# Kernel tuning notes

Measured on AMD Instinct MI355X. Metric: run time of the kernel, lower is better.

## Reference

```python
import jax, jax.numpy as jnp
import numpy as np

S = 2        # downscale
REDUCE = 32  # QK channel dim


def _to_grid(x):
    # [B,C,H,W] -> [B,C,H/S,W/S,S*S], matching ConverToGrid (reshape+permute+reshape)
    B, C, H, W = x.shape
    h, w = H // S, W // S
    x = x.reshape(B, C, h, S, w, S)
    x = x.transpose(0, 1, 2, 4, 3, 5)
    return x.reshape(B, C, h, w, S * S)


def setup_inputs() -> dict:
    key = jax.random.key(0)
    k1, k2, k3 = jax.random.split(key, 3)
    fm = jax.random.normal(k1, (8, 128, 256, 256), dtype=jnp.float32)
    Wq = jax.random.normal(k2, (REDUCE, 128), dtype=jnp.float32) * 0.05
    Wk = jax.random.normal(k3, (REDUCE, 128), dtype=jnp.float32) * 0.05
    return {"fm": fm, "Wq": Wq, "Wk": Wk}


def reference(fm, Wq, Wk):
    B, C, H, W = fm.shape
    h, w = H // S, W // S
    # Q branch: AvgPool2d(S,S) -> 1x1 conv -> scale by 1/sqrt(reduce)
    pooled = fm.reshape(B, C, h, S, w, S).mean(axis=(3, 5))          # [B,C,h,w]
    Q = jnp.einsum('rc,bchw->brhw', Wq, pooled) / jnp.sqrt(
        jnp.asarray(REDUCE, fm.dtype))                               # [B,r,h,w]
    # K branch: 1x1 conv -> grid
    K = _to_grid(jnp.einsum('rc,bchw->brhw', Wk, fm))                # [B,r,h,w,S*S]
    # V branch: grid of raw features
    V = _to_grid(fm)                                                 # [B,C,h,w,S*S]
    # sum over channel dim of Q*K, softmax over window dim (dropout p=0 => identity)
    logits = jnp.einsum('brhw,brhws->bhws', Q, K)                    # [B,h,w,S*S]
    attn = jax.nn.softmax(logits, axis=-1)
    # weighted sum over window positions
    out = jnp.einsum('bchws,bhws->bchw', V, attn)                    # [B,C,h,w]
    return out
```

## Files before the change

### kernel.cpp

```cpp
#include <hip/hip_runtime.h>
#include <math.h>


__global__ __launch_bounds__(256) void wt_kernel(const float* __restrict__ Wq,
                                                 const float* __restrict__ Wk,
                                                 float* __restrict__ ws) {
  int t = blockIdx.x * 256 + threadIdx.x;
  if (t < 4096) {
    int c = t >> 5, r = t & 31;
    ws[c * 32 + r]        = Wq[r * 128 + c] * (0.25f / sqrtf(32.0f));
    ws[4096 + c * 32 + r] = Wk[r * 128 + c];
  }
}

__global__ __launch_bounds__(256, 8)
void attn_main(const float* __restrict__ fm,
               const float* __restrict__ ws,
               float* __restrict__ out) {
  __shared__ float Qpart[32 * 128];
  __shared__ float lbuf[2 * 128 * 4];

  const int tid  = threadIdx.x;
  const int p    = tid & 127;
  const int half = __builtin_amdgcn_readfirstlane(tid >> 7);
  const int blk  = blockIdx.x;
  const int h    = blk & 127;
  const int b    = blk >> 7;
  const int cbase = half * 64;

  const float* gbase = fm + ((size_t)(b * 128 + cbase) * 65536) +
                       (size_t)(2 * h) * 256 + 2 * p;
  const float* wq = ws + cbase * 32;
  const float* wk = ws + 4096 + cbase * 32;

  float qa[32];
#pragma unroll
  for (int r = 0; r < 32; ++r) qa[r] = 0.f;
  {
    const float* g = gbase;
#pragma unroll 4
    for (int i = 0; i < 64; ++i) {
      const float2 va = *(const float2*)(g);
      const float2 vb = *(const float2*)(g + 256);
      const float u = (va.x + va.y) + (vb.x + vb.y);
#pragma unroll
      for (int r = 0; r < 32; ++r)
        qa[r] = fmaf(wq[i * 32 + r], u, qa[r]);
      g += 65536;
    }
  }
  if (half == 1) {
#pragma unroll
    for (int r = 0; r < 32; ++r) Qpart[r * 128 + p] = qa[r];
  }
  __syncthreads();
  if (half == 0) {
#pragma unroll
    for (int r = 0; r < 32; ++r) {
      const float t = qa[r] + Qpart[r * 128 + p];
      qa[r] = t;
      Qpart[r * 128 + p] = t;
    }
  }
  __syncthreads();
  if (half == 1) {
#pragma unroll
    for (int r = 0; r < 32; ++r) qa[r] = Qpart[r * 128 + p];
  }

  float l0 = 0.f, l1 = 0.f, l2 = 0.f, l3 = 0.f;
  {
    const float* g = gbase + (size_t)63 * 65536;
#pragma unroll 2
    for (int i = 63; i >= 0; --i) {
      const float2 va = *(const float2*)(g);
      const float2 vb = *(const float2*)(g + 256);
      float t0 = 0.f, t1 = 0.f, t2 = 0.f, t3 = 0.f;
#pragma unroll
      for (int r = 0; r < 32; r += 4) {
        t0 = fmaf(qa[r + 0], wk[i * 32 + r + 0], t0);
        t1 = fmaf(qa[r + 1], wk[i * 32 + r + 1], t1);
        t2 = fmaf(qa[r + 2], wk[i * 32 + r + 2], t2);
        t3 = fmaf(qa[r + 3], wk[i * 32 + r + 3], t3);
      }
      const float tv = (t0 + t1) + (t2 + t3);
      l0 = fmaf(tv, va.x, l0);
      l1 = fmaf(tv, va.y, l1);
      l2 = fmaf(tv, vb.x, l2);
      l3 = fmaf(tv, vb.y, l3);
      g -= 65536;
    }
  }
  *(float4*)(lbuf + (half * 128 + p) * 4) = make_float4(l0, l1, l2, l3);
  __syncthreads();

  if (half == 0) {
    const float4 o = *(const float4*)(lbuf + (128 + p) * 4);
    const float L0 = l0 + o.x, L1 = l1 + o.y, L2 = l2 + o.z, L3 = l3 + o.w;
    const float mx = fmaxf(fmaxf(L0, L1), fmaxf(L2, L3));
    const float e0 = __expf(L0 - mx), e1 = __expf(L1 - mx);
    const float e2 = __expf(L2 - mx), e3 = __expf(L3 - mx);
    const float inv = 1.0f / ((e0 + e1) + (e2 + e3));
    *(float4*)(lbuf + p * 4) =
        make_float4(e0 * inv, e1 * inv, e2 * inv, e3 * inv);
  }
  __syncthreads();
  const float4 at = *(const float4*)(lbuf + p * 4);

  {
    const float* g = gbase;
    float* op = out + ((size_t)(b * 128 + cbase) * 16384) + h * 128 + p;
#pragma unroll 8
    for (int i = 0; i < 64; ++i) {
      const float2 va = *(const float2*)(g);
      const float2 vb = *(const float2*)(g + 256);
      const float o =
          fmaf(at.x, va.x, fmaf(at.y, va.y, fmaf(at.z, vb.x, at.w * vb.y)));
      __builtin_nontemporal_store(o, op);
      g += 65536;
      op += 16384;
    }
  }
}

extern "C" void kernel_launch(void* const* d_in, const int* in_sizes, int n_in,
                              void* d_out, int out_size, void* d_ws, size_t ws_size,
                              hipStream_t stream) {
  const float* fm = (const float*)d_in[0];
  const float* Wq = (const float*)d_in[1];
  const float* Wk = (const float*)d_in[2];
  float* outp = (float*)d_out;
  float* ws = (float*)d_ws;

  wt_kernel<<<16, 256, 0, stream>>>(Wq, Wk, ws);
  attn_main<<<1024, 256, 0, stream>>>(fm, ws, outp);
}
```

Measured before the change: 149.0 us.

## Split channels over four waves per block and halve row width per block

Each block now covers half a pooled row (64 columns) with four wavefronts, each owning 32 channels instead of 64. The grid doubles to 2048 blocks, and the Q and logit partial sums are reduced across four groups in shared memory. The channel loops are manually unrolled by four so several independent loads are in flight, which aims to raise memory-level parallelism and occupancy for this bandwidth-bound kernel. In exchange there is more reduction traffic through shared memory, and each wave's row segment is shorter, so global accesses are less contiguous.

```diff
diff --git a/kernel.cpp b/kernel.cpp
--- a/kernel.cpp
+++ b/kernel.cpp
@@ -17,86 +17,119 @@
 void attn_main(const float* __restrict__ fm,
                const float* __restrict__ ws,
                float* __restrict__ out) {
-  __shared__ float Qpart[32 * 128];
-  __shared__ float lbuf[2 * 128 * 4];
+  __shared__ float Qpart[2 * 32 * 64];
+  __shared__ float lbuf[4 * 64 * 4];
 
-  const int tid  = threadIdx.x;
-  const int p    = tid & 127;
-  const int half = __builtin_amdgcn_readfirstlane(tid >> 7);
-  const int blk  = blockIdx.x;
-  const int h    = blk & 127;
-  const int b    = blk >> 7;
-  const int cbase = half * 64;
+  const int tid = threadIdx.x;
+  const int p   = tid & 63;
+  const int grp = __builtin_amdgcn_readfirstlane(tid >> 6);
 
-  const float* gbase = fm + ((size_t)(b * 128 + cbase) * 65536) +
-                       (size_t)(2 * h) * 256 + 2 * p;
-  const float* wq = ws + cbase * 32;
-  const float* wk = ws + 4096 + cbase * 32;
+  const int blk = blockIdx.x;
+  const int w0  = (blk & 1) * 64;
+  const int h   = (blk >> 1) & 127;
+  const int b   = blk >> 8;
+  const int cb  = grp * 32;
+
+  const float* gbase = fm + ((size_t)(b * 128 + cb) * 65536) +
+                       (size_t)(2 * h) * 256 + 2 * (w0 + p);
+  const float* wq = ws + cb * 32;
+  const float* wk = ws + 4096 + cb * 32;
 
   float qa[32];
 #pragma unroll
   for (int r = 0; r < 32; ++r) qa[r] = 0.f;
   {
     const float* g = gbase;
-#pragma unroll 4
-    for (int i = 0; i < 64; ++i) {
-      const float2 va = *(const float2*)(g);
-      const float2 vb = *(const float2*)(g + 256);
-      const float u = (va.x + va.y) + (vb.x + vb.y);
+#pragma unroll 2
+    for (int i0 = 0; i0 < 32; i0 += 4) {
+      const float2 va0 = *(const float2*)(g + 0 * 65536);
+      const float2 vb0 = *(const float2*)(g + 0 * 65536 + 256);
+      const float2 va1 = *(const float2*)(g + 1 * 65536);
+      const float2 vb1 = *(const float2*)(g + 1 * 65536 + 256);
+      const float2 va2 = *(const float2*)(g + 2 * 65536);
+      const float2 vb2 = *(const float2*)(g + 2 * 65536 + 256);
+      const float2 va3 = *(const float2*)(g + 3 * 65536);
+      const float2 vb3 = *(const float2*)(g + 3 * 65536 + 256);
+      const float u0 = (va0.x + va0.y) + (vb0.x + vb0.y);
+      const float u1 = (va1.x + va1.y) + (vb1.x + vb1.y);
+      const float u2 = (va2.x + va2.y) + (vb2.x + vb2.y);
+      const float u3 = (va3.x + va3.y) + (vb3.x + vb3.y);
 #pragma unroll
-      for (int r = 0; r < 32; ++r)
-        qa[r] = fmaf(wq[i * 32 + r], u, qa[r]);
-      g += 65536;
+      for (int r = 0; r < 32; ++r) {
+        float acc = qa[r];
+        acc = fmaf(wq[(i0 + 0) * 32 + r], u0, acc);
+        acc = fmaf(wq[(i0 + 1) * 32 + r], u1, acc);
+        acc = fmaf(wq[(i0 + 2) * 32 + r], u2, acc);
+        acc = fmaf(wq[(i0 + 3) * 32 + r], u3, acc);
+        qa[r] = acc;
+      }
+      g += 4 * 65536;
     }
   }
-  if (half == 1) {
+
+  if (grp >= 2) {
 #pragma unroll
-    for (int r = 0; r < 32; ++r) Qpart[r * 128 + p] = qa[r];
+    for (int r = 0; r < 32; ++r) Qpart[(grp - 2) * 2048 + r * 64 + p] = qa[r];
   }
   __syncthreads();
-  if (half == 0) {
+  if (grp < 2) {
 #pragma unroll
     for (int r = 0; r < 32; ++r) {
-      const float t = qa[r] + Qpart[r * 128 + p];
-      qa[r] = t;
-      Qpart[r * 128 + p] = t;
+      const float t = qa[r] + Qpart[grp * 2048 + r * 64 + p];
+      Qpart[grp * 2048 + r * 64 + p] = t;
     }
   }
   __syncthreads();
-  if (half == 1) {
 #pragma unroll
-    for (int r = 0; r < 32; ++r) qa[r] = Qpart[r * 128 + p];
-  }
+  for (int r = 0; r < 32; ++r)
+    qa[r] = Qpart[r * 64 + p] + Qpart[2048 + r * 64 + p];
 
   float l0 = 0.f, l1 = 0.f, l2 = 0.f, l3 = 0.f;
   {
-    const float* g = gbase + (size_t)63 * 65536;
+    const float* g = gbase + (size_t)28 * 65536;
 #pragma unroll 2
-    for (int i = 63; i >= 0; --i) {
-      const float2 va = *(const float2*)(g);
-      const float2 vb = *(const float2*)(g + 256);
-      float t0 = 0.f, t1 = 0.f, t2 = 0.f, t3 = 0.f;
+    for (int i0 = 28; i0 >= 0; i0 -= 4) {
+      const float2 va0 = *(const float2*)(g + 0 * 65536);
+      const float2 vb0 = *(const float2*)(g + 0 * 65536 + 256);
+      const float2 va1 = *(const float2*)(g + 1 * 65536);
+      const float2 vb1 = *(const float2*)(g + 1 * 65536 + 256);
+      const float2 va2 = *(const float2*)(g + 2 * 65536);
+      const float2 vb2 = *(const float2*)(g + 2 * 65536 + 256);
+      const float2 va3 = *(const float2*)(g + 3 * 65536);
+      const float2 vb3 = *(const float2*)(g + 3 * 65536 + 256);
 #pragma unroll
-      for (int r = 0; r < 32; r += 4) {
-        t0 = fmaf(qa[r + 0], wk[i * 32 + r + 0], t0);
-        t1 = fmaf(qa[r + 1], wk[i * 32 + r + 1], t1);
-        t2 = fmaf(qa[r + 2], wk[i * 32 + r + 2], t2);
-        t3 = fmaf(qa[r + 3], wk[i * 32 + r + 3], t3);
+      for (int j = 0; j < 4; ++j) {
+        const int c = i0 + j;
+        float t0 = 0.f, t1 = 0.f, t2 = 0.f, t3 = 0.f;
+#pragma unroll
+        for (int r = 0; r < 32; r += 4) {
+          t0 = fmaf(qa[r + 0], wk[c * 32 + r + 0], t0);
+          t1 = fmaf(qa[r + 1], wk[c * 32 + r + 1], t1);
+          t2 = fmaf(qa[r + 2], wk[c * 32 + r + 2], t2);
+          t3 = fmaf(qa[r + 3], wk[c * 32 + r + 3], t3);
+        }
+        const float tv = (t0 + t1) + (t2 + t3);
+        const float2 va = (j == 0) ? va0 : (j == 1) ? va1 : (j == 2) ? va2 : va3;
+        const float2 vb = (j == 0) ? vb0 : (j == 1) ? vb1 : (j == 2) ? vb2 : vb3;
+        l0 = fmaf(tv, va.x, l0);
+        l1 = fmaf(tv, va.y, l1);
+        l2 = fmaf(tv, vb.x, l2);
+        l3 = fmaf(tv, vb.y, l3);
       }
-      const float tv = (t0 + t1) + (t2 + t3);
-      l0 = fmaf(tv, va.x, l0);
-      l1 = fmaf(tv, va.y, l1);
-      l2 = fmaf(tv, vb.x, l2);
-      l3 = fmaf(tv, vb.y, l3);
-      g -= 65536;
+      g -= 4 * 65536;
     }
   }
-  *(float4*)(lbuf + (half * 128 + p) * 4) = make_float4(l0, l1, l2, l3);
+  *(float4*)(lbuf + (grp * 64 + p) * 4) = make_float4(l0, l1, l2, l3);
   __syncthreads();
 
-  if (half == 0) {
-    const float4 o = *(const float4*)(lbuf + (128 + p) * 4);
-    const float L0 = l0 + o.x, L1 = l1 + o.y, L2 = l2 + o.z, L3 = l3 + o.w;
+  if (grp == 0) {
+    const float4 o1 = *(const float4*)(lbuf + (64 + p) * 4);
+    const float4 o2 = *(const float4*)(lbuf + (128 + p) * 4);
+    const float4 o3 = *(const float4*)(lbuf + (192 + p) * 4);
+    const float L0 = (l0 + o1.x) + (o2.x + o3.x);
+    const float L1 = (l1 + o1.y) + (o2.y + o3.y);
+    const float L2 = (l2 + o1.z) + (o2.z + o3.z);
+    const float L3 = (l3 + o1.w) + (o2.w + o3.w);
     const float mx = fmaxf(fmaxf(L0, L1), fmaxf(L2, L3));
     const float e0 = __expf(L0 - mx), e1 = __expf(L1 - mx);
     const float e2 = __expf(L2 - mx), e3 = __expf(L3 - mx);
@@ -109,16 +142,27 @@
 
   {
     const float* g = gbase;
-    float* op = out + ((size_t)(b * 128 + cbase) * 16384) + h * 128 + p;
-#pragma unroll 8
-    for (int i = 0; i < 64; ++i) {
-      const float2 va = *(const float2*)(g);
-      const float2 vb = *(const float2*)(g + 256);
-      const float o =
-          fmaf(at.x, va.x, fmaf(at.y, va.y, fmaf(at.z, vb.x, at.w * vb.y)));
-      __builtin_nontemporal_store(o, op);
-      g += 65536;
-      op += 16384;
+    float* op = out + ((size_t)(b * 128 + cb) * 16384) + h * 128 + w0 + p;
+#pragma unroll 2
+    for (int i0 = 0; i0 < 32; i0 += 4) {
+      const float2 va0 = *(const float2*)(g + 0 * 65536);
+      const float2 vb0 = *(const float2*)(g + 0 * 65536 + 256);
+      const float2 va1 = *(const float2*)(g + 1 * 65536);
+      const float2 vb1 = *(const float2*)(g + 1 * 65536 + 256);
+      const float2 va2 = *(const float2*)(g + 2 * 65536);
+      const float2 vb2 = *(const float2*)(g + 2 * 65536 + 256);
+      const float2 va3 = *(const float2*)(g + 3 * 65536);
+      const float2 vb3 = *(const float2*)(g + 3 * 65536 + 256);
+      const float o0 = fmaf(at.x, va0.x, fmaf(at.y, va0.y, fmaf(at.z, vb0.x, at.w * vb0.y)));
+      const float o1 = fmaf(at.x, va1.x, fmaf(at.y, va1.y, fmaf(at.z, vb1.x, at.w * vb1.y)));
+      const float o2 = fmaf(at.x, va2.x, fmaf(at.y, va2.y, fmaf(at.z, vb2.x, at.w * vb2.y)));
+      const float o3 = fmaf(at.x, va3.x, fmaf(at.y, va3.y, fmaf(at.z, vb3.x, at.w * vb3.y)));
+      __builtin_nontemporal_store(o0, op);
+      __builtin_nontemporal_store(o1, op + 16384);
+      __builtin_nontemporal_store(o2, op + 2 * 16384);
+      __builtin_nontemporal_store(o3, op + 3 * 16384);
+      g += 4 * 65536;
+      op += 4 * 16384;
     }
   }
 }
@@ -133,5 +177,5 @@
   float* ws = (float*)d_ws;
 
   wt_kernel<<<16, 256, 0, stream>>>(Wq, Wk, ws);
-  attn_main<<<1024, 256, 0, stream>>>(fm, ws, outp);
+  attn_main<<<2048, 256, 0, stream>>>(fm, ws, outp);
 }
```

Result: no change. 146.4 us (-1.8%).

## Cache input tile in registers as packed bf16 to read fm once

Applied to the files above, without the earlier changes.

Each thread now loads its fm window values once, packs them into bf16 register pairs, and reuses them for the Q pooling, the logit accumulation and the final weighted sum, instead of reading global memory three times. Work is split across four 32-channel wave groups per 64-pixel tile with a doubled grid and a reduced occupancy hint. This trades global/L2 traffic for higher register use and bf16 rounding of V and logits inputs, which may affect accuracy. The nontemporal output store is also dropped.

```diff
diff --git a/kernel.cpp b/kernel.cpp
--- a/kernel.cpp
+++ b/kernel.cpp
@@ -1,6 +1,21 @@
 #include <hip/hip_runtime.h>
+#include <hip/hip_bf16.h>
 #include <math.h>
 
+
+typedef unsigned int uint32;
+
+__device__ __forceinline__ uint32 pack2(float x, float y) {
+  union { __hip_bfloat162 h; uint32 u; } cvt;
+  cvt.h = __float22bfloat162_rn(make_float2(x, y));
+  return cvt.u;
+}
+__device__ __forceinline__ float2 unpack2(uint32 u) {
+  float2 r;
+  r.x = __uint_as_float(u << 16);
+  r.y = __uint_as_float(u & 0xffff0000u);
+  return r;
+}
 
 __global__ __launch_bounds__(256) void wt_kernel(const float* __restrict__ Wq,
                                                  const float* __restrict__ Wk,
@@ -13,90 +28,98 @@
   }
 }
 
-__global__ __launch_bounds__(256, 8)
+__global__ __launch_bounds__(256, 4)
 void attn_main(const float* __restrict__ fm,
                const float* __restrict__ ws,
                float* __restrict__ out) {
-  __shared__ float Qpart[32 * 128];
-  __shared__ float lbuf[2 * 128 * 4];
+  __shared__ float Qpart[2 * 32 * 64];
+  __shared__ float lbuf[4 * 64 * 4];
 
-  const int tid  = threadIdx.x;
-  const int p    = tid & 127;
-  const int half = __builtin_amdgcn_readfirstlane(tid >> 7);
-  const int blk  = blockIdx.x;
-  const int h    = blk & 127;
-  const int b    = blk >> 7;
-  const int cbase = half * 64;
+  const int tid = threadIdx.x;
+  const int p   = tid & 63;
+  const int grp = __builtin_amdgcn_readfirstlane(tid >> 6);
 
-  const float* gbase = fm + ((size_t)(b * 128 + cbase) * 65536) +
-                       (size_t)(2 * h) * 256 + 2 * p;
-  const float* wq = ws + cbase * 32;
-  const float* wk = ws + 4096 + cbase * 32;
+  const int blk = blockIdx.x;
+  const int w0  = (blk & 1) * 64;
+  const int h   = (blk >> 1) & 127;
+  const int b   = blk >> 8;
+  const int cb  = grp * 32;
+
+  const float* gbase = fm + ((size_t)(b * 128 + cb) * 65536) +
+                       (size_t)(2 * h) * 256 + 2 * (w0 + p);
+  const float* wq = ws + cb * 32;
+  const float* wk = ws + 4096 + cb * 32;
+
+  uint32 pka[32], pkb[32];
+  {
+    const float* g = gbase;
+#pragma unroll
+    for (int i = 0; i < 32; ++i) {
+      const float2 va = *(const float2*)(g);
+      const float2 vb = *(const float2*)(g + 256);
+      pka[i] = pack2(va.x, va.y);
+      pkb[i] = pack2(vb.x, vb.y);
+      g += 65536;
+    }
+  }
 
   float qa[32];
 #pragma unroll
   for (int r = 0; r < 32; ++r) qa[r] = 0.f;
-  {
-    const float* g = gbase;
-#pragma unroll 4
-    for (int i = 0; i < 64; ++i) {
-      const float2 va = *(const float2*)(g);
-      const float2 vb = *(const float2*)(g + 256);
-      const float u = (va.x + va.y) + (vb.x + vb.y);
 #pragma unroll
-      for (int r = 0; r < 32; ++r)
-        qa[r] = fmaf(wq[i * 32 + r], u, qa[r]);
-      g += 65536;
-    }
+  for (int i = 0; i < 32; ++i) {
+    const float2 va = unpack2(pka[i]);
+    const float2 vb = unpack2(pkb[i]);
+    const float u = (va.x + va.y) + (vb.x + vb.y);
+#pragma unroll
+    for (int r = 0; r < 32; ++r)
+      qa[r] = fmaf(wq[i * 32 + r], u, qa[r]);
   }
-  if (half == 1) {
+
+  if (grp >= 2) {
 #pragma unroll
-    for (int r = 0; r < 32; ++r) Qpart[r * 128 + p] = qa[r];
+    for (int r = 0; r < 32; ++r) Qpart[(grp - 2) * 2048 + r * 64 + p] = qa[r];
   }
   __syncthreads();
-  if (half == 0) {
+  if (grp < 2) {
 #pragma unroll
-    for (int r = 0; r < 32; ++r) {
-      const float t = qa[r] + Qpart[r * 128 + p];
-      qa[r] = t;
-      Qpart[r * 128 + p] = t;
-    }
+    for (int r = 0; r < 32; ++r) Qpart[grp * 2048 + r * 64 + p] += qa[r];
   }
   __syncthreads();
-  if (half == 1) {
 #pragma unroll
-    for (int r = 0; r < 32; ++r) qa[r] = Qpart[r * 128 + p];
-  }
+  for (int r = 0; r < 32; ++r)
+    qa[r] = Qpart[r * 64 + p] + Qpart[2048 + r * 64 + p];
 
   float l0 = 0.f, l1 = 0.f, l2 = 0.f, l3 = 0.f;
-  {
-    const float* g = gbase + (size_t)63 * 65536;
-#pragma unroll 2
-    for (int i = 63; i >= 0; --i) {
-      const float2 va = *(const float2*)(g);
-      const float2 vb = *(const float2*)(g + 256);
-      float t0 = 0.f, t1 = 0.f, t2 = 0.f, t3 = 0.f;
 #pragma unroll
-      for (int r = 0; r < 32; r += 4) {
-        t0 = fmaf(qa[r + 0], wk[i * 32 + r + 0], t0);
-        t1 = fmaf(qa[r + 1], wk[i * 32 + r + 1], t1);
-        t2 = fmaf(qa[r + 2], wk[i * 32 + r + 2], t2);
-        t3 = fmaf(qa[r + 3], wk[i * 32 + r + 3], t3);
-      }
-      const float tv = (t0 + t1) + (t2 + t3);
-      l0 = fmaf(tv, va.x, l0);
-      l1 = fmaf(tv, va.y, l1);
-      l2 = fmaf(tv, vb.x, l2);
-      l3 = fmaf(tv, vb.y, l3);
-      g -= 65536;
+  for (int i = 0; i < 32; ++i) {
+    const float2 va = unpack2(pka[i]);
+    const float2 vb = unpack2(pkb[i]);
+    float t0 = 0.f, t1 = 0.f, t2 = 0.f, t3 = 0.f;
+#pragma unroll
+    for (int r = 0; r < 32; r += 4) {
+      t0 = fmaf(qa[r + 0], wk[i * 32 + r + 0], t0);
+      t1 = fmaf(qa[r + 1], wk[i * 32 + r + 1], t1);
+      t2 = fmaf(qa[r + 2], wk[i * 32 + r + 2], t2);
+      t3 = fmaf(qa[r + 3], wk[i * 32 + r + 3], t3);
     }
+    const float tv = (t0 + t1) + (t2 + t3);
+    l0 = fmaf(tv, va.x, l0);
+    l1 = fmaf(tv, va.y, l1);
+    l2 = fmaf(tv, vb.x, l2);
+    l3 = fmaf(tv, vb.y, l3);
   }
-  *(float4*)(lbuf + (half * 128 + p) * 4) = make_float4(l0, l1, l2, l3);
+  *(float4*)(lbuf + (grp * 64 + p) * 4) = make_float4(l0, l1, l2, l3);
   __syncthreads();
 
-  if (half == 0) {
-    const float4 o = *(const float4*)(lbuf + (128 + p) * 4);
-    const float L0 = l0 + o.x, L1 = l1 + o.y, L2 = l2 + o.z, L3 = l3 + o.w;
+  if (grp == 0) {
+    const float4 o1 = *(const float4*)(lbuf + (64 + p) * 4);
+    const float4 o2 = *(const float4*)(lbuf + (128 + p) * 4);
+    const float4 o3 = *(const float4*)(lbuf + (192 + p) * 4);
+    const float L0 = (l0 + o1.x) + (o2.x + o3.x);
+    const float L1 = (l1 + o1.y) + (o2.y + o3.y);
+    const float L2 = (l2 + o1.z) + (o2.z + o3.z);
+    const float L3 = (l3 + o1.w) + (o2.w + o3.w);
     const float mx = fmaxf(fmaxf(L0, L1), fmaxf(L2, L3));
     const float e0 = __expf(L0 - mx), e1 = __expf(L1 - mx);
     const float e2 = __expf(L2 - mx), e3 = __expf(L3 - mx);
@@ -108,17 +131,13 @@
   const float4 at = *(const float4*)(lbuf + p * 4);
 
   {
-    const float* g = gbase;
-    float* op = out + ((size_t)(b * 128 + cbase) * 16384) + h * 128 + p;
-#pragma unroll 8
-    for (int i = 0; i < 64; ++i) {
-      const float2 va = *(const float2*)(g);
-      const float2 vb = *(const float2*)(g + 256);
-      const float o =
+    float* op = out + ((size_t)(b * 128 + cb) * 16384) + h * 128 + w0 + p;
+#pragma unroll
+    for (int i = 0; i < 32; ++i) {
+      const float2 va = unpack2(pka[i]);
+      const float2 vb = unpack2(pkb[i]);
+      op[(size_t)i * 16384] =
           fmaf(at.x, va.x, fmaf(at.y, va.y, fmaf(at.z, vb.x, at.w * vb.y)));
-      __builtin_nontemporal_store(o, op);
-      g += 65536;
-      op += 16384;
     }
   }
 }
@@ -133,5 +152,5 @@
   float* ws = (float*)d_ws;
 
   wt_kernel<<<16, 256, 0, stream>>>(Wq, Wk, ws);
-  attn_main<<<1024, 256, 0, stream>>>(fm, ws, outp);
+  attn_main<<<2048, 256, 0, stream>>>(fm, ws, outp);
 }
```

Result: slower. 157.9 us (+5.9%).
